# Optimization experiments

Measured on AMD Instinct MI355X. Metric: run time of the kernel, lower is better.

Reference implementation:

```python
import jax, jax.numpy as jnp
import numpy as np

B, T, C = 4, 4096, 1024
ATT_SCALE = 1.0
TIME_MIX_RATIO = 1.0


def setup_inputs() -> dict:
    key = jax.random.key(0)
    ks = jax.random.split(key, 7)
    std = 0.02  # 0.02 * (layer_id + 1), layer_id = 0
    x = jax.random.normal(ks[0], (B, T, C), dtype=jnp.float32)
    state = jnp.zeros((B, C), dtype=jnp.float32)
    W_r = jax.random.normal(ks[1], (C, C), dtype=jnp.float32) * std
    W_k = jax.random.normal(ks[2], (C, C), dtype=jnp.float32) * std
    W_v = jax.random.normal(ks[3], (C, C), dtype=jnp.float32) * std
    W_o = jax.random.normal(ks[4], (C, C), dtype=jnp.float32) * std
    time_mix_r = jnp.ones((1, 1, C), dtype=jnp.float32) * TIME_MIX_RATIO
    time_mix_k = jnp.ones((1, 1, C), dtype=jnp.float32) * TIME_MIX_RATIO
    time_mix_v = jnp.ones((1, 1, C), dtype=jnp.float32) * TIME_MIX_RATIO
    # learned log-decay; use negative values so exp(time_decay) < 1 and the
    # recurrence is numerically stable over T=4096 steps (a trained model
    # would have such values; the torch init 0.9 would blow up for long T)
    time_decay = jax.random.uniform(ks[5], (C,), dtype=jnp.float32,
                                    minval=-0.1, maxval=-0.01)
    return {"x": x, "state": state, "W_r": W_r, "W_k": W_k, "W_v": W_v,
            "W_o": W_o, "time_mix_r": time_mix_r, "time_mix_k": time_mix_k,
            "time_mix_v": time_mix_v, "time_decay": time_decay}


def reference(x, state, W_r, W_k, W_v, W_o,
              time_mix_r, time_mix_k, time_mix_v, time_decay):
    # shifted input: previous-token stream, seeded with incoming state
    x_mix = jnp.concatenate([state[:, None, :], x[:, :-1]], axis=1)  # [B,T,C]

    r_in = x * time_mix_r + x_mix * (1.0 - time_mix_r)
    k_in = x * time_mix_k + x_mix * (1.0 - time_mix_k)
    v_in = x * time_mix_v + x_mix * (1.0 - time_mix_v)

    r = jax.nn.sigmoid(jnp.einsum('btc,dc->btd', r_in, W_r))
    k = jnp.exp(jnp.einsum('btc,dc->btd', k_in, W_k))
    v = jnp.einsum('btc,dc->btd', v_in, W_v)

    decay = jnp.exp(time_decay)  # [C]
    kv = k * v                   # [B,T,C]

    def step(s, inp):
        kv_t, r_t = inp          # each [B,C]
        s = s * decay + kv_t
        return s, r_t * s

    _, out = jax.lax.scan(step, state,
                          (kv.transpose(1, 0, 2), r.transpose(1, 0, 2)))
    out = out.transpose(1, 0, 2) * ATT_SCALE          # [B,T,C]

    output = jnp.einsum('btc,dc->btd', out, W_o)      # time_output
    new_state = x[:, -1]
    return output, new_state
```

## Files before the change

kernel.cpp:

```cpp
#include <hip/hip_runtime.h>

#define B_ 4
#define T_ 4096
#define C_ 1024
#define M_ (B_*T_)
#define BTC (B_*T_*C_)
#define NCHUNK 64
#define CHUNK (T_ / NCHUNK)

typedef unsigned short u16;
typedef __attribute__((ext_vector_type(8))) short bf16x8;
typedef __attribute__((ext_vector_type(4))) float f32x4;

static __device__ __forceinline__ u16 f2bf(float f) {
    unsigned u = __float_as_uint(f);
    unsigned r = (u + 0x7FFFu + ((u >> 16) & 1u)) >> 16;
    return (u16)r;
}
static __device__ __forceinline__ float bf2f(u16 h) {
    return __uint_as_float(((unsigned)h) << 16);
}

__global__ void prep_kernel(const float* __restrict__ x, const float* __restrict__ state,
                            const float* __restrict__ tmr, const float* __restrict__ tmk,
                            const float* __restrict__ tmv,
                            u16* __restrict__ rin, u16* __restrict__ kin, u16* __restrict__ vin,
                            float* __restrict__ new_state) {
    int idx4 = blockIdx.x * blockDim.x + threadIdx.x;
    const int n4 = BTC / 4;
    if (idx4 >= n4) return;
    const int C4 = C_ / 4;
    int c4 = idx4 % C4;
    int bt = idx4 / C4;
    int t  = bt % T_;
    int b  = bt / T_;
    float4 xc = ((const float4*)x)[idx4];
    float4 xp = (t == 0) ? ((const float4*)state)[b * C4 + c4]
                         : ((const float4*)x)[idx4 - C4];
    float4 mr = ((const float4*)tmr)[c4];
    float4 mk = ((const float4*)tmk)[c4];
    float4 mv = ((const float4*)tmv)[c4];
    ushort4 pr, pk, pv;
    pr.x = f2bf(xc.x*mr.x + xp.x*(1.f-mr.x));
    pr.y = f2bf(xc.y*mr.y + xp.y*(1.f-mr.y));
    pr.z = f2bf(xc.z*mr.z + xp.z*(1.f-mr.z));
    pr.w = f2bf(xc.w*mr.w + xp.w*(1.f-mr.w));
    pk.x = f2bf(xc.x*mk.x + xp.x*(1.f-mk.x));
    pk.y = f2bf(xc.y*mk.y + xp.y*(1.f-mk.y));
    pk.z = f2bf(xc.z*mk.z + xp.z*(1.f-mk.z));
    pk.w = f2bf(xc.w*mk.w + xp.w*(1.f-mk.w));
    pv.x = f2bf(xc.x*mv.x + xp.x*(1.f-mv.x));
    pv.y = f2bf(xc.y*mv.y + xp.y*(1.f-mv.y));
    pv.z = f2bf(xc.z*mv.z + xp.z*(1.f-mv.z));
    pv.w = f2bf(xc.w*mv.w + xp.w*(1.f-mv.w));
    ((ushort4*)rin)[idx4] = pr;
    ((ushort4*)kin)[idx4] = pk;
    ((ushort4*)vin)[idx4] = pv;
    if (t == T_ - 1) ((float4*)new_state)[b * C4 + c4] = xc;
}

__global__ void cast_all_kernel(const float* __restrict__ w0, const float* __restrict__ w1,
                                const float* __restrict__ w2, const float* __restrict__ w3,
                                u16* __restrict__ dst) {
    int w = blockIdx.x >> 10;
    int i = ((blockIdx.x & 1023) << 8) + threadIdx.x;
    const float* src = (w == 0) ? w0 : (w == 1) ? w1 : (w == 2) ? w2 : w3;
    float4 v = ((const float4*)src)[i];
    ushort4 o;
    o.x = f2bf(v.x); o.y = f2bf(v.y); o.z = f2bf(v.z); o.w = f2bf(v.w);
    ((ushort4*)(dst + (size_t)w * C_ * C_))[i] = o;
}

#define EPI_SIG  0
#define EPI_EXP  1
#define EPI_BF16 2
#define EPI_F32  3

template <int EPI>
__global__ __launch_bounds__(512, 2)
void gemm256(const u16* __restrict__ A, const u16* __restrict__ W,
             void* __restrict__ Cptr, int M, int N, int K) {
    extern __shared__ __align__(16) u16 smem[];
    u16* sA = smem;
    u16* sB = smem + 2 * 256 * 64;

    const int tid  = threadIdx.x;
    const int wid  = tid >> 6, lane = tid & 63;
    const int wr   = wid >> 2, wc = wid & 3;
    const int lr   = lane & 15, kq = lane >> 4;

    const int wg   = blockIdx.x;
    const int wgid = (wg & 7) * 32 + (wg >> 3);
    const int bm   = wgid >> 2, bn = wgid & 3;
    const int row0 = bm * 256, col0 = bn * 256;
    const int nk   = K / 64;

    f32x4 acc[8][4];
#pragma unroll
    for (int i = 0; i < 8; ++i)
#pragma unroll
        for (int j = 0; j < 4; ++j)
#pragma unroll
            for (int q = 0; q < 4; ++q) acc[i][j][q] = 0.f;

    const int rl = tid >> 3;
    const int uu = tid & 7;
    const int usw = uu ^ (rl & 7);

    auto stA = [&](int buf, int h, int kt) {
#pragma unroll
        for (int p = 0; p < 2; ++p) {
            int r  = p * 64 + rl;
            int rt = h * 128 + r;
            const u16* g = A + (size_t)(row0 + rt) * K + kt * 64 + usw * 8;
            __builtin_amdgcn_global_load_lds(
                (const __attribute__((address_space(1))) void*)g,
                (__attribute__((address_space(3))) void*)&sA[buf * 16384 + rt * 64 + uu * 8],
                16, 0, 0);
        }
    };
    auto stB = [&](int buf, int h, int kt) {
#pragma unroll
        for (int p = 0; p < 2; ++p) {
            int r  = p * 64 + rl;
            int rt = h * 128 + r;
            const u16* g = W + (size_t)(col0 + rt) * K + kt * 64 + usw * 8;
            __builtin_amdgcn_global_load_lds(
                (const __attribute__((address_space(1))) void*)g,
                (__attribute__((address_space(3))) void*)&sB[buf * 16384 + rt * 64 + uu * 8],
                16, 0, 0);
        }
    };
    auto ldA = [&](int buf, int ig, int ks) -> bf16x8 {
        int R = wr * 128 + ig * 16 + lr;
        int unit = (ks * 4 + kq) ^ (lr & 7);
        return *(const bf16x8*)&sA[buf * 16384 + R * 64 + unit * 8];
    };
    auto ldB = [&](int buf, int j, int ks) -> bf16x8 {
        int R = wc * 64 + j * 16 + lr;
        int unit = (ks * 4 + kq) ^ (lr & 7);
        return *(const bf16x8*)&sB[buf * 16384 + R * 64 + unit * 8];
    };

    stA(0, 0, 0); stA(0, 1, 0); stB(0, 0, 0); stB(0, 1, 0);
    stB(1, 0, 1); stB(1, 1, 1);
    asm volatile("s_waitcnt vmcnt(4)" ::: "memory");
    __builtin_amdgcn_s_barrier();

    for (int kt = 0; kt < nk; ++kt) {
        const int cur = kt & 1, nxt = cur ^ 1;
        const int t1 = (kt + 1 < nk) ? kt + 1 : nk - 1;
        const int t2 = (kt + 2 < nk) ? kt + 2 : nk - 1;

        bf16x8 b[4][2];
        bf16x8 a0[2][2];
#pragma unroll
        for (int j = 0; j < 4; ++j)
#pragma unroll
            for (int ks = 0; ks < 2; ++ks) b[j][ks] = ldB(cur, j, ks);
#pragma unroll
        for (int i = 0; i < 2; ++i)
#pragma unroll
            for (int ks = 0; ks < 2; ++ks) a0[i][ks] = ldA(cur, i, ks);
        stA(nxt, 0, t1);
        __builtin_amdgcn_sched_barrier(0);
        __builtin_amdgcn_s_setprio(1);
#pragma unroll
        for (int i = 0; i < 2; ++i)
#pragma unroll
            for (int j = 0; j < 4; ++j)
#pragma unroll
                for (int ks = 0; ks < 2; ++ks)
                    acc[i][j] = __builtin_amdgcn_mfma_f32_16x16x32_bf16(a0[i][ks], b[j][ks], acc[i][j], 0, 0, 0);
        __builtin_amdgcn_s_setprio(0);
        __builtin_amdgcn_s_barrier();

        bf16x8 a1[2][2];
#pragma unroll
        for (int i = 0; i < 2; ++i)
#pragma unroll
            for (int ks = 0; ks < 2; ++ks) a1[i][ks] = ldA(cur, 2 + i, ks);
        stA(nxt, 1, t1);
        __builtin_amdgcn_sched_barrier(0);
        __builtin_amdgcn_s_setprio(1);
#pragma unroll
        for (int i = 0; i < 2; ++i)
#pragma unroll
            for (int j = 0; j < 4; ++j)
#pragma unroll
                for (int ks = 0; ks < 2; ++ks)
                    acc[2 + i][j] = __builtin_amdgcn_mfma_f32_16x16x32_bf16(a1[i][ks], b[j][ks], acc[2 + i][j], 0, 0, 0);
        __builtin_amdgcn_s_setprio(0);
        __builtin_amdgcn_s_barrier();

        bf16x8 a2[2][2];
#pragma unroll
        for (int i = 0; i < 2; ++i)
#pragma unroll
            for (int ks = 0; ks < 2; ++ks) a2[i][ks] = ldA(cur, 4 + i, ks);
        stB(cur, 0, t2);
        __builtin_amdgcn_sched_barrier(0);
        __builtin_amdgcn_s_setprio(1);
#pragma unroll
        for (int i = 0; i < 2; ++i)
#pragma unroll
            for (int j = 0; j < 4; ++j)
#pragma unroll
                for (int ks = 0; ks < 2; ++ks)
                    acc[4 + i][j] = __builtin_amdgcn_mfma_f32_16x16x32_bf16(a2[i][ks], b[j][ks], acc[4 + i][j], 0, 0, 0);
        __builtin_amdgcn_s_setprio(0);
        __builtin_amdgcn_s_barrier();

        bf16x8 a3[2][2];
#pragma unroll
        for (int i = 0; i < 2; ++i)
#pragma unroll
            for (int ks = 0; ks < 2; ++ks) a3[i][ks] = ldA(cur, 6 + i, ks);
        stB(cur, 1, t2);
        __builtin_amdgcn_sched_barrier(0);
        __builtin_amdgcn_s_setprio(1);
#pragma unroll
        for (int i = 0; i < 2; ++i)
#pragma unroll
            for (int j = 0; j < 4; ++j)
#pragma unroll
                for (int ks = 0; ks < 2; ++ks)
                    acc[6 + i][j] = __builtin_amdgcn_mfma_f32_16x16x32_bf16(a3[i][ks], b[j][ks], acc[6 + i][j], 0, 0, 0);
        __builtin_amdgcn_s_setprio(0);
        asm volatile("s_waitcnt vmcnt(4)" ::: "memory");
        __builtin_amdgcn_s_barrier();
    }

    const int r0 = row0 + wr * 128;
    const int c0 = col0 + wc * 64;
#pragma unroll
    for (int i = 0; i < 8; ++i) {
#pragma unroll
        for (int j = 0; j < 4; ++j) {
#pragma unroll
            for (int q = 0; q < 4; ++q) {
                int rr = r0 + i * 16 + kq * 4 + q;
                int cc = c0 + j * 16 + lr;
                float v = acc[i][j][q];
                size_t o = (size_t)rr * N + cc;
                if constexpr (EPI == EPI_SIG) {
                    ((u16*)Cptr)[o] = f2bf(1.0f / (1.0f + __expf(-v)));
                } else if constexpr (EPI == EPI_EXP) {
                    ((u16*)Cptr)[o] = f2bf(__expf(v));
                } else if constexpr (EPI == EPI_BF16) {
                    ((u16*)Cptr)[o] = f2bf(v);
                } else {
                    ((float*)Cptr)[o] = v;
                }
            }
        }
    }
}

__global__ void scan_partial(const u16* __restrict__ ek, const u16* __restrict__ vv,
                             const float* __restrict__ td, float* __restrict__ S) {
    const int tid = threadIdx.x;
    const int bid = blockIdx.x;
    const int ct  = bid & 3;
    const int j   = (bid >> 2) & (NCHUNK - 1);
    const int b   = bid >> 8;
    const int c   = ct * 256 + tid;
    const float d = __expf(td[c]);
    float s = 0.f;
    size_t base = ((size_t)(b * T_ + j * CHUNK)) * C_ + c;
#pragma unroll 4
    for (int t = 0; t < CHUNK; ++t) {
        size_t ix = base + (size_t)t * C_;
        s = s * d + bf2f(ek[ix]) * bf2f(vv[ix]);
    }
    S[((size_t)(b * NCHUNK + j)) * C_ + c] = s;
}

__global__ void scan_carry(const float* __restrict__ S, const float* __restrict__ td,
                           const float* __restrict__ state, float* __restrict__ carry) {
    int id = blockIdx.x * blockDim.x + threadIdx.x;
    if (id >= B_ * C_) return;
    int c = id & (C_ - 1);
    int b = id >> 10;
    float dl = __expf(td[c] * (float)CHUNK);
    float E = state[id];
#pragma unroll 8
    for (int j = 0; j < NCHUNK; ++j) {
        size_t o = ((size_t)(b * NCHUNK + j)) * C_ + c;
        carry[o] = E;
        E = dl * E + S[o];
    }
}

__global__ void scan_apply(const u16* __restrict__ ek, const u16* __restrict__ vv,
                           const u16* __restrict__ rr, const float* __restrict__ td,
                           const float* __restrict__ carry, u16* __restrict__ out) {
    const int tid = threadIdx.x;
    const int bid = blockIdx.x;
    const int ct  = bid & 3;
    const int j   = (bid >> 2) & (NCHUNK - 1);
    const int b   = bid >> 8;
    const int c   = ct * 256 + tid;
    const float d = __expf(td[c]);
    float s = carry[((size_t)(b * NCHUNK + j)) * C_ + c];
    size_t base = ((size_t)(b * T_ + j * CHUNK)) * C_ + c;
#pragma unroll 4
    for (int t = 0; t < CHUNK; ++t) {
        size_t ix = base + (size_t)t * C_;
        s = s * d + bf2f(ek[ix]) * bf2f(vv[ix]);
        out[ix] = f2bf(s * bf2f(rr[ix]));
    }
}

extern "C" void kernel_launch(void* const* d_in, const int* in_sizes, int n_in,
                              void* d_out, int out_size, void* d_ws, size_t ws_size,
                              hipStream_t stream) {
    const float* x     = (const float*)d_in[0];
    const float* state = (const float*)d_in[1];
    const float* W_r   = (const float*)d_in[2];
    const float* W_k   = (const float*)d_in[3];
    const float* W_v   = (const float*)d_in[4];
    const float* W_o   = (const float*)d_in[5];
    const float* tmr   = (const float*)d_in[6];
    const float* tmk   = (const float*)d_in[7];
    const float* tmv   = (const float*)d_in[8];
    const float* td    = (const float*)d_in[9];

    float* out_f     = (float*)d_out;
    float* new_state = out_f + (size_t)BTC;

    char* ws = (char*)d_ws;
    const size_t SZ = (size_t)BTC * 2;
    u16* rin   = (u16*)(ws + 0 * SZ);
    u16* kin   = (u16*)(ws + 1 * SZ);
    u16* vin   = (u16*)(ws + 2 * SZ);
    u16* rbuf  = (u16*)(ws + 3 * SZ);
    u16* ekbuf = (u16*)(ws + 4 * SZ);
    u16* vbuf  = (u16*)(ws + 5 * SZ);
    u16* wts   = (u16*)(ws + 6 * SZ);
    u16* wrb   = wts;
    u16* wkb   = wrb + (size_t)C_ * C_;
    u16* wvb   = wkb + (size_t)C_ * C_;
    u16* wob   = wvb + (size_t)C_ * C_;
    float* Sbuf  = (float*)(wob + (size_t)C_ * C_);
    float* cbuf  = Sbuf + (size_t)B_ * NCHUNK * C_;
    u16* outb  = vin;

    prep_kernel<<<(BTC / 4 + 255) / 256, 256, 0, stream>>>(
        x, state, tmr, tmk, tmv, rin, kin, vin, new_state);

    cast_all_kernel<<<4096, 256, 0, stream>>>(W_r, W_k, W_v, W_o, wts);

    const dim3 gg(256);
    const int LDSB = 2 * 2 * 256 * 64 * 2;
    gemm256<EPI_SIG ><<<gg, 512, LDSB, stream>>>(rin, wrb, (void*)rbuf,  M_, C_, C_);
    gemm256<EPI_EXP ><<<gg, 512, LDSB, stream>>>(kin, wkb, (void*)ekbuf, M_, C_, C_);
    gemm256<EPI_BF16><<<gg, 512, LDSB, stream>>>(vin, wvb, (void*)vbuf,  M_, C_, C_);

    const int nscan_blocks = B_ * NCHUNK * (C_ / 256);
    scan_partial<<<nscan_blocks, 256, 0, stream>>>(ekbuf, vbuf, td, Sbuf);
    scan_carry<<<(B_ * C_ + 255) / 256, 256, 0, stream>>>(Sbuf, td, state, cbuf);
    scan_apply<<<nscan_blocks, 256, 0, stream>>>(ekbuf, vbuf, rbuf, td, cbuf, outb);

    gemm256<EPI_F32><<<gg, 512, LDSB, stream>>>(outb, wob, (void*)out_f, M_, C_, C_);
}
```

Before: 243.2 us.

## Batch R/K/V GEMMs into one launch, use 32x32x16 MFMA, widen prep vectors

```diff
diff --git a/kernel.cpp b/kernel.cpp
--- a/kernel.cpp
+++ b/kernel.cpp
@@ -10,7 +10,9 @@
 
 typedef unsigned short u16;
 typedef __attribute__((ext_vector_type(8))) short bf16x8;
+typedef __attribute__((ext_vector_type(8))) unsigned short u16x8;
 typedef __attribute__((ext_vector_type(4))) float f32x4;
+typedef __attribute__((ext_vector_type(16))) float f32x16;
 
 static __device__ __forceinline__ u16 f2bf(float f) {
     unsigned u = __float_as_uint(f);
@@ -26,37 +28,45 @@
                             const float* __restrict__ tmv,
                             u16* __restrict__ rin, u16* __restrict__ kin, u16* __restrict__ vin,
                             float* __restrict__ new_state) {
-    int idx4 = blockIdx.x * blockDim.x + threadIdx.x;
-    const int n4 = BTC / 4;
-    if (idx4 >= n4) return;
-    const int C4 = C_ / 4;
-    int c4 = idx4 % C4;
-    int bt = idx4 / C4;
-    int t  = bt % T_;
-    int b  = bt / T_;
-    float4 xc = ((const float4*)x)[idx4];
-    float4 xp = (t == 0) ? ((const float4*)state)[b * C4 + c4]
-                         : ((const float4*)x)[idx4 - C4];
-    float4 mr = ((const float4*)tmr)[c4];
-    float4 mk = ((const float4*)tmk)[c4];
-    float4 mv = ((const float4*)tmv)[c4];
-    ushort4 pr, pk, pv;
-    pr.x = f2bf(xc.x*mr.x + xp.x*(1.f-mr.x));
-    pr.y = f2bf(xc.y*mr.y + xp.y*(1.f-mr.y));
-    pr.z = f2bf(xc.z*mr.z + xp.z*(1.f-mr.z));
-    pr.w = f2bf(xc.w*mr.w + xp.w*(1.f-mr.w));
-    pk.x = f2bf(xc.x*mk.x + xp.x*(1.f-mk.x));
-    pk.y = f2bf(xc.y*mk.y + xp.y*(1.f-mk.y));
-    pk.z = f2bf(xc.z*mk.z + xp.z*(1.f-mk.z));
-    pk.w = f2bf(xc.w*mk.w + xp.w*(1.f-mk.w));
-    pv.x = f2bf(xc.x*mv.x + xp.x*(1.f-mv.x));
-    pv.y = f2bf(xc.y*mv.y + xp.y*(1.f-mv.y));
-    pv.z = f2bf(xc.z*mv.z + xp.z*(1.f-mv.z));
-    pv.w = f2bf(xc.w*mv.w + xp.w*(1.f-mv.w));
-    ((ushort4*)rin)[idx4] = pr;
-    ((ushort4*)kin)[idx4] = pk;
-    ((ushort4*)vin)[idx4] = pv;
-    if (t == T_ - 1) ((float4*)new_state)[b * C4 + c4] = xc;
+    const int idx = blockIdx.x * 256 + threadIdx.x;
+    const int c8 = idx & 127;
+    const int bt = idx >> 7;
+    const int t  = bt & (T_ - 1);
+    const int b  = bt >> 12;
+
+    const float4* xv = (const float4*)x;
+    float4 xa = xv[idx * 2], xb = xv[idx * 2 + 1];
+    float4 pa, pb;
+    if (t == 0) {
+        const float4* sv = (const float4*)state;
+        pa = sv[(b * 128 + c8) * 2]; pb = sv[(b * 128 + c8) * 2 + 1];
+    } else {
+        pa = xv[(idx - 128) * 2]; pb = xv[(idx - 128) * 2 + 1];
+    }
+    float4 mra = ((const float4*)tmr)[c8 * 2], mrb = ((const float4*)tmr)[c8 * 2 + 1];
+    float4 mka = ((const float4*)tmk)[c8 * 2], mkb = ((const float4*)tmk)[c8 * 2 + 1];
+    float4 mva = ((const float4*)tmv)[c8 * 2], mvb = ((const float4*)tmv)[c8 * 2 + 1];
+
+    float xc[8] = {xa.x, xa.y, xa.z, xa.w, xb.x, xb.y, xb.z, xb.w};
+    float xp[8] = {pa.x, pa.y, pa.z, pa.w, pb.x, pb.y, pb.z, pb.w};
+    float mr[8] = {mra.x, mra.y, mra.z, mra.w, mrb.x, mrb.y, mrb.z, mrb.w};
+    float mk[8] = {mka.x, mka.y, mka.z, mka.w, mkb.x, mkb.y, mkb.z, mkb.w};
+    float mv[8] = {mva.x, mva.y, mva.z, mva.w, mvb.x, mvb.y, mvb.z, mvb.w};
+
+    u16x8 pr, pk, pv;
+#pragma unroll
+    for (int j = 0; j < 8; ++j) {
+        pr[j] = f2bf(xc[j] * mr[j] + xp[j] * (1.f - mr[j]));
+        pk[j] = f2bf(xc[j] * mk[j] + xp[j] * (1.f - mk[j]));
+        pv[j] = f2bf(xc[j] * mv[j] + xp[j] * (1.f - mv[j]));
+    }
+    ((u16x8*)rin)[idx] = pr;
+    ((u16x8*)kin)[idx] = pk;
+    ((u16x8*)vin)[idx] = pv;
+    if (t == T_ - 1) {
+        ((float4*)new_state)[(b * 128 + c8) * 2]     = xa;
+        ((float4*)new_state)[(b * 128 + c8) * 2 + 1] = xb;
+    }
 }
 
 __global__ void cast_all_kernel(const float* __restrict__ w0, const float* __restrict__ w1,
@@ -76,32 +86,39 @@
 #define EPI_BF16 2
 #define EPI_F32  3
 
-template <int EPI>
 __global__ __launch_bounds__(512, 2)
-void gemm256(const u16* __restrict__ A, const u16* __restrict__ W,
-             void* __restrict__ Cptr, int M, int N, int K) {
+void gemm256(const u16* __restrict__ A0, const u16* __restrict__ A1, const u16* __restrict__ A2,
+             const u16* __restrict__ Wb, void* __restrict__ C0, void* __restrict__ C1,
+             void* __restrict__ C2, int epis) {
     extern __shared__ __align__(16) u16 smem[];
     u16* sA = smem;
     u16* sB = smem + 2 * 256 * 64;
 
+    const int id = blockIdx.x >> 8;
+    const int wg = blockIdx.x & 255;
+    const u16* A = (id == 0) ? A0 : (id == 1) ? A1 : A2;
+    const u16* W = Wb + (size_t)id * C_ * C_;
+    void* Cptr   = (id == 0) ? C0 : (id == 1) ? C1 : C2;
+    const int epi = (epis >> (id * 8)) & 255;
+
     const int tid  = threadIdx.x;
     const int wid  = tid >> 6, lane = tid & 63;
     const int wr   = wid >> 2, wc = wid & 3;
-    const int lr   = lane & 15, kq = lane >> 4;
-
-    const int wg   = blockIdx.x;
+    const int l31  = lane & 31, kh = lane >> 5;
+
     const int wgid = (wg & 7) * 32 + (wg >> 3);
     const int bm   = wgid >> 2, bn = wgid & 3;
     const int row0 = bm * 256, col0 = bn * 256;
+    const int K    = C_;
     const int nk   = K / 64;
 
-    f32x4 acc[8][4];
-#pragma unroll
-    for (int i = 0; i < 8; ++i)
-#pragma unroll
-        for (int j = 0; j < 4; ++j)
-#pragma unroll
-            for (int q = 0; q < 4; ++q) acc[i][j][q] = 0.f;
+    f32x16 acc[4][2];
+#pragma unroll
+    for (int i = 0; i < 4; ++i)
+#pragma unroll
+        for (int j = 0; j < 2; ++j)
+#pragma unroll
+            for (int q = 0; q < 16; ++q) acc[i][j][q] = 0.f;
 
     const int rl = tid >> 3;
     const int uu = tid & 7;
@@ -110,8 +127,7 @@
     auto stA = [&](int buf, int h, int kt) {
 #pragma unroll
         for (int p = 0; p < 2; ++p) {
-            int r  = p * 64 + rl;
-            int rt = h * 128 + r;
+            int rt = h * 128 + p * 64 + rl;
             const u16* g = A + (size_t)(row0 + rt) * K + kt * 64 + usw * 8;
             __builtin_amdgcn_global_load_lds(
                 (const __attribute__((address_space(1))) void*)g,
@@ -122,8 +138,7 @@
     auto stB = [&](int buf, int h, int kt) {
 #pragma unroll
         for (int p = 0; p < 2; ++p) {
-            int r  = p * 64 + rl;
-            int rt = h * 128 + r;
+            int rt = h * 128 + p * 64 + rl;
             const u16* g = W + (size_t)(col0 + rt) * K + kt * 64 + usw * 8;
             __builtin_amdgcn_global_load_lds(
                 (const __attribute__((address_space(1))) void*)g,
@@ -131,14 +146,14 @@
                 16, 0, 0);
         }
     };
-    auto ldA = [&](int buf, int ig, int ks) -> bf16x8 {
-        int R = wr * 128 + ig * 16 + lr;
-        int unit = (ks * 4 + kq) ^ (lr & 7);
+    auto ldA = [&](int buf, int rt, int ks) -> bf16x8 {
+        int R = wr * 128 + rt * 32 + l31;
+        int unit = (ks * 2 + kh) ^ (l31 & 7);
         return *(const bf16x8*)&sA[buf * 16384 + R * 64 + unit * 8];
     };
-    auto ldB = [&](int buf, int j, int ks) -> bf16x8 {
-        int R = wc * 64 + j * 16 + lr;
-        int unit = (ks * 4 + kq) ^ (lr & 7);
+    auto ldB = [&](int buf, int ct, int ks) -> bf16x8 {
+        int R = wc * 64 + ct * 32 + l31;
+        int unit = (ks * 2 + kh) ^ (l31 & 7);
         return *(const bf16x8*)&sB[buf * 16384 + R * 64 + unit * 8];
     };
 
@@ -152,102 +167,91 @@
         const int t1 = (kt + 1 < nk) ? kt + 1 : nk - 1;
         const int t2 = (kt + 2 < nk) ? kt + 2 : nk - 1;
 
-        bf16x8 b[4][2];
-        bf16x8 a0[2][2];
-#pragma unroll
-        for (int j = 0; j < 4; ++j)
-#pragma unroll
-            for (int ks = 0; ks < 2; ++ks) b[j][ks] = ldB(cur, j, ks);
-#pragma unroll
-        for (int i = 0; i < 2; ++i)
-#pragma unroll
-            for (int ks = 0; ks < 2; ++ks) a0[i][ks] = ldA(cur, i, ks);
-        stA(nxt, 0, t1);
-        __builtin_amdgcn_sched_barrier(0);
-        __builtin_amdgcn_s_setprio(1);
-#pragma unroll
-        for (int i = 0; i < 2; ++i)
-#pragma unroll
-            for (int j = 0; j < 4; ++j)
-#pragma unroll
-                for (int ks = 0; ks < 2; ++ks)
-                    acc[i][j] = __builtin_amdgcn_mfma_f32_16x16x32_bf16(a0[i][ks], b[j][ks], acc[i][j], 0, 0, 0);
-        __builtin_amdgcn_s_setprio(0);
-        __builtin_amdgcn_s_barrier();
-
-        bf16x8 a1[2][2];
-#pragma unroll
-        for (int i = 0; i < 2; ++i)
-#pragma unroll
-            for (int ks = 0; ks < 2; ++ks) a1[i][ks] = ldA(cur, 2 + i, ks);
-        stA(nxt, 1, t1);
-        __builtin_amdgcn_sched_barrier(0);
-        __builtin_amdgcn_s_setprio(1);
-#pragma unroll
-        for (int i = 0; i < 2; ++i)
-#pragma unroll
-            for (int j = 0; j < 4; ++j)
-#pragma unroll
-                for (int ks = 0; ks < 2; ++ks)
-                    acc[2 + i][j] = __builtin_amdgcn_mfma_f32_16x16x32_bf16(a1[i][ks], b[j][ks], acc[2 + i][j], 0, 0, 0);
-        __builtin_amdgcn_s_setprio(0);
-        __builtin_amdgcn_s_barrier();
-
-        bf16x8 a2[2][2];
-#pragma unroll
-        for (int i = 0; i < 2; ++i)
-#pragma unroll
-            for (int ks = 0; ks < 2; ++ks) a2[i][ks] = ldA(cur, 4 + i, ks);
-        stB(cur, 0, t2);
-        __builtin_amdgcn_sched_barrier(0);
-        __builtin_amdgcn_s_setprio(1);
-#pragma unroll
-        for (int i = 0; i < 2; ++i)
-#pragma unroll
-            for (int j = 0; j < 4; ++j)
-#pragma unroll
-                for (int ks = 0; ks < 2; ++ks)
-                    acc[4 + i][j] = __builtin_amdgcn_mfma_f32_16x16x32_bf16(a2[i][ks], b[j][ks], acc[4 + i][j], 0, 0, 0);
-        __builtin_amdgcn_s_setprio(0);
-        __builtin_amdgcn_s_barrier();
-
-        bf16x8 a3[2][2];
-#pragma unroll
-        for (int i = 0; i < 2; ++i)
-#pragma unroll
-            for (int ks = 0; ks < 2; ++ks) a3[i][ks] = ldA(cur, 6 + i, ks);
-        stB(cur, 1, t2);
-        __builtin_amdgcn_sched_barrier(0);
-        __builtin_amdgcn_s_setprio(1);
-#pragma unroll
-        for (int i = 0; i < 2; ++i)
-#pragma unroll
-            for (int j = 0; j < 4; ++j)
-#pragma unroll
-                for (int ks = 0; ks < 2; ++ks)
-                    acc[6 + i][j] = __builtin_amdgcn_mfma_f32_16x16x32_bf16(a3[i][ks], b[j][ks], acc[6 + i][j], 0, 0, 0);
-        __builtin_amdgcn_s_setprio(0);
-        asm volatile("s_waitcnt vmcnt(4)" ::: "memory");
-        __builtin_amdgcn_s_barrier();
+        bf16x8 b[2][4];
+        {
+            bf16x8 a[4];
+#pragma unroll
+            for (int ct = 0; ct < 2; ++ct)
+#pragma unroll
+                for (int ks = 0; ks < 4; ++ks) b[ct][ks] = ldB(cur, ct, ks);
+#pragma unroll
+            for (int ks = 0; ks < 4; ++ks) a[ks] = ldA(cur, 0, ks);
+            stA(nxt, 0, t1);
+            __builtin_amdgcn_sched_barrier(0);
+            __builtin_amdgcn_s_setprio(1);
+#pragma unroll
+            for (int ks = 0; ks < 4; ++ks)
+#pragma unroll
+                for (int ct = 0; ct < 2; ++ct)
+                    acc[0][ct] = __builtin_amdgcn_mfma_f32_32x32x16_bf16(a[ks], b[ct][ks], acc[0][ct], 0, 0, 0);
+            __builtin_amdgcn_s_setprio(0);
+            __builtin_amdgcn_s_barrier();
+        }
+        {
+            bf16x8 a[4];
+#pragma unroll
+            for (int ks = 0; ks < 4; ++ks) a[ks] = ldA(cur, 1, ks);
+            stA(nxt, 1, t1);
+            __builtin_amdgcn_sched_barrier(0);
+            __builtin_amdgcn_s_setprio(1);
+#pragma unroll
+            for (int ks = 0; ks < 4; ++ks)
+#pragma unroll
+                for (int ct = 0; ct < 2; ++ct)
+                    acc[1][ct] = __builtin_amdgcn_mfma_f32_32x32x16_bf16(a[ks], b[ct][ks], acc[1][ct], 0, 0, 0);
+            __builtin_amdgcn_s_setprio(0);
+            __builtin_amdgcn_s_barrier();
+        }
+        {
+            bf16x8 a[4];
+#pragma unroll
+            for (int ks = 0; ks < 4; ++ks) a[ks] = ldA(cur, 2, ks);
+            stB(cur, 0, t2);
+            __builtin_amdgcn_sched_barrier(0);
+            __builtin_amdgcn_s_setprio(1);
+#pragma unroll
+            for (int ks = 0; ks < 4; ++ks)
+#pragma unroll
+                for (int ct = 0; ct < 2; ++ct)
+                    acc[2][ct] = __builtin_amdgcn_mfma_f32_32x32x16_bf16(a[ks], b[ct][ks], acc[2][ct], 0, 0, 0);
+            __builtin_amdgcn_s_setprio(0);
+            __builtin_amdgcn_s_barrier();
+        }
+        {
+            bf16x8 a[4];
+#pragma unroll
+            for (int ks = 0; ks < 4; ++ks) a[ks] = ldA(cur, 3, ks);
+            stB(cur, 1, t2);
+            __builtin_amdgcn_sched_barrier(0);
+            __builtin_amdgcn_s_setprio(1);
+#pragma unroll
+            for (int ks = 0; ks < 4; ++ks)
+#pragma unroll
+                for (int ct = 0; ct < 2; ++ct)
+                    acc[3][ct] = __builtin_amdgcn_mfma_f32_32x32x16_bf16(a[ks], b[ct][ks], acc[3][ct], 0, 0, 0);
+            __builtin_amdgcn_s_setprio(0);
+            asm volatile("s_waitcnt vmcnt(4)" ::: "memory");
+            __builtin_amdgcn_s_barrier();
+        }
     }
 
     const int r0 = row0 + wr * 128;
     const int c0 = col0 + wc * 64;
 #pragma unroll
-    for (int i = 0; i < 8; ++i) {
-#pragma unroll
-        for (int j = 0; j < 4; ++j) {
-#pragma unroll
-            for (int q = 0; q < 4; ++q) {
-                int rr = r0 + i * 16 + kq * 4 + q;
-                int cc = c0 + j * 16 + lr;
-                float v = acc[i][j][q];
-                size_t o = (size_t)rr * N + cc;
-                if constexpr (EPI == EPI_SIG) {
+    for (int rt = 0; rt < 4; ++rt) {
+#pragma unroll
+        for (int ct = 0; ct < 2; ++ct) {
+#pragma unroll
+            for (int q = 0; q < 16; ++q) {
+                int rr = r0 + rt * 32 + (q & 3) + 8 * (q >> 2) + 4 * kh;
+                int cc = c0 + ct * 32 + l31;
+                float v = acc[rt][ct][q];
+                size_t o = (size_t)rr * C_ + cc;
+                if (epi == EPI_SIG) {
                     ((u16*)Cptr)[o] = f2bf(1.0f / (1.0f + __expf(-v)));
-                } else if constexpr (EPI == EPI_EXP) {
+                } else if (epi == EPI_EXP) {
                     ((u16*)Cptr)[o] = f2bf(__expf(v));
-                } else if constexpr (EPI == EPI_BF16) {
+                } else if (epi == EPI_BF16) {
                     ((u16*)Cptr)[o] = f2bf(v);
                 } else {
                     ((float*)Cptr)[o] = v;
@@ -339,28 +343,26 @@
     u16* vbuf  = (u16*)(ws + 5 * SZ);
     u16* wts   = (u16*)(ws + 6 * SZ);
     u16* wrb   = wts;
-    u16* wkb   = wrb + (size_t)C_ * C_;
-    u16* wvb   = wkb + (size_t)C_ * C_;
-    u16* wob   = wvb + (size_t)C_ * C_;
+    u16* wob   = wts + 3 * (size_t)C_ * C_;
     float* Sbuf  = (float*)(wob + (size_t)C_ * C_);
     float* cbuf  = Sbuf + (size_t)B_ * NCHUNK * C_;
     u16* outb  = vin;
 
-    prep_kernel<<<(BTC / 4 + 255) / 256, 256, 0, stream>>>(
+    prep_kernel<<<BTC / 8 / 256, 256, 0, stream>>>(
         x, state, tmr, tmk, tmv, rin, kin, vin, new_state);
 
     cast_all_kernel<<<4096, 256, 0, stream>>>(W_r, W_k, W_v, W_o, wts);
 
-    const dim3 gg(256);
     const int LDSB = 2 * 2 * 256 * 64 * 2;
-    gemm256<EPI_SIG ><<<gg, 512, LDSB, stream>>>(rin, wrb, (void*)rbuf,  M_, C_, C_);
-    gemm256<EPI_EXP ><<<gg, 512, LDSB, stream>>>(kin, wkb, (void*)ekbuf, M_, C_, C_);
-    gemm256<EPI_BF16><<<gg, 512, LDSB, stream>>>(vin, wvb, (void*)vbuf,  M_, C_, C_);
+    const int epis3 = EPI_SIG | (EPI_EXP << 8) | (EPI_BF16 << 16);
+    gemm256<<<768, 512, LDSB, stream>>>(rin, kin, vin, wrb,
+                                        (void*)rbuf, (void*)ekbuf, (void*)vbuf, epis3);
 
     const int nscan_blocks = B_ * NCHUNK * (C_ / 256);
     scan_partial<<<nscan_blocks, 256, 0, stream>>>(ekbuf, vbuf, td, Sbuf);
     scan_carry<<<(B_ * C_ + 255) / 256, 256, 0, stream>>>(Sbuf, td, state, cbuf);
     scan_apply<<<nscan_blocks, 256, 0, stream>>>(ekbuf, vbuf, rbuf, td, cbuf, outb);
 
-    gemm256<EPI_F32><<<gg, 512, LDSB, stream>>>(outb, wob, (void*)out_f, M_, C_, C_);
-}
+    gemm256<<<256, 512, LDSB, stream>>>(outb, outb, outb, wob,
+                                        (void*)out_f, (void*)out_f, (void*)out_f, EPI_F32);
+}
```

Measured after the change: 266.9 us. 9.8% more time.
